# Kernel tuning notes

Measured on AMD Instinct MI355X. Metric: run time of the kernel, lower is better.

## Reference

```python
import jax, jax.numpy as jnp
import numpy as np

B, T, DIM = 2, 2048, 1024
HID = 4096
H, KVH, HD = 16, 4, 64
WIN = 512
NORM_EPS = 1e-5
QK_EPS = 1e-6
LS_INIT = 0.01


def setup_inputs() -> dict:
    key = jax.random.key(0)
    ks = jax.random.split(key, 12)
    s = lambda fan_in: 1.0 / np.sqrt(fan_in)
    return {
        "x": jax.random.normal(ks[0], (B, T, DIM), jnp.float32),
        # torch Linear weights are (out, in); y = x @ W.T
        "wq": jax.random.normal(ks[1], (H * HD, DIM), jnp.float32) * s(DIM),
        "wk": jax.random.normal(ks[2], (KVH * HD, DIM), jnp.float32) * s(DIM),
        "wv": jax.random.normal(ks[3], (KVH * HD, DIM), jnp.float32) * s(DIM),
        "wo": jax.random.normal(ks[4], (DIM, H * HD), jnp.float32) * s(H * HD),
        "w1": jax.random.normal(ks[5], (HID, DIM), jnp.float32) * s(DIM),
        "w2": jax.random.normal(ks[6], (DIM, HID), jnp.float32) * s(HID),
        "w3": jax.random.normal(ks[7], (HID, DIM), jnp.float32) * s(DIM),
        "q_norm_w": jnp.ones((HD,), jnp.float32),
        "k_norm_w": jnp.ones((HD,), jnp.float32),
        "attn_norm_w": jnp.ones((DIM,), jnp.float32),
        "ffn_norm_w": jnp.ones((DIM,), jnp.float32),
        "attn_scale": jnp.full((DIM,), LS_INIT, jnp.float32),
        "ffn_scale": jnp.full((DIM,), LS_INIT, jnp.float32),
    }


def _rmsnorm(x, w, eps):
    return x * jax.lax.rsqrt(jnp.mean(x * x, axis=-1, keepdims=True) + eps) * w


def _attention(x, wq, wk, wv, wo, q_norm_w, k_norm_w):
    b, t, _ = x.shape
    q = (x @ wq.T).reshape(b, t, H, HD)
    k = (x @ wk.T).reshape(b, t, KVH, HD)
    v = (x @ wv.T).reshape(b, t, KVH, HD)
    q = _rmsnorm(q, q_norm_w, QK_EPS)
    k = _rmsnorm(k, k_norm_w, QK_EPS)
    # GQA: repeat kv heads to H heads
    rep = H // KVH
    k = jnp.repeat(k, rep, axis=2)  # (b,t,H,HD)
    v = jnp.repeat(v, rep, axis=2)
    scale = 1.0 / np.sqrt(HD)
    scores = jnp.einsum("bqhd,bkhd->bhqk", q, k) * scale  # (b,H,t,t)
    row = jnp.arange(t)[:, None]
    col = jnp.arange(t)[None, :]
    mask = (row >= col) & (row - col < WIN)  # (t,t) bool
    scores = jnp.where(mask[None, None], scores, -jnp.inf)
    probs = jax.nn.softmax(scores, axis=-1)
    y = jnp.einsum("bhqk,bkhd->bqhd", probs, v).reshape(b, t, H * HD)
    return y @ wo.T


def reference(x, wq, wk, wv, wo, w1, w2, w3, q_norm_w, k_norm_w,
              attn_norm_w, ffn_norm_w, attn_scale, ffn_scale):
    r = _attention(_rmsnorm(x, attn_norm_w, NORM_EPS), wq, wk, wv, wo,
                   q_norm_w, k_norm_w)
    h = x + r * attn_scale
    hn = _rmsnorm(h, ffn_norm_w, NORM_EPS)
    ffn = (jax.nn.silu(hn @ w1.T) * (hn @ w3.T)) @ w2.T
    return h + ffn * ffn_scale
```

## Files before the change

kernel.cpp:

```cpp
#include <hip/hip_runtime.h>

typedef unsigned short u16;
typedef unsigned int u32;
typedef unsigned char u8;
typedef short bf16x8 __attribute__((ext_vector_type(8)));
typedef float f32x4 __attribute__((ext_vector_type(4)));
typedef float f32x16 __attribute__((ext_vector_type(16)));
typedef int i32x4 __attribute__((ext_vector_type(4)));
typedef int i32x8 __attribute__((ext_vector_type(8)));

#define AS1 __attribute__((address_space(1)))
#define AS3 __attribute__((address_space(3)))

#define B_ 2
#define T_ 2048
#define DIM_ 1024
#define HID_ 4096
#define H_ 16
#define KVH_ 4
#define HD_ 64
#define WIN_ 512

#define SCALE_A 0x7C7C7C7C
#define SCALE_B 0x79797979

__device__ __forceinline__ u16 f2bf(float f) {
    union { float f; u32 u; } v; v.f = f;
    u32 r = v.u + 0x7FFFu + ((v.u >> 16) & 1u);
    return (u16)(r >> 16);
}
__device__ __forceinline__ float bf2f(u32 u) {
    union { u32 u; float f; } v; v.u = u << 16;
    return v.f;
}
__device__ __forceinline__ float4 ld4bf(const u16* p) {
    uint2 u = *(const uint2*)p;
    float4 r;
    r.x = bf2f(u.x & 0xFFFFu); r.y = bf2f(u.x >> 16);
    r.z = bf2f(u.y & 0xFFFFu); r.w = bf2f(u.y >> 16);
    return r;
}
__device__ __forceinline__ void load_lds16(const void* g, void* l) {
    __builtin_amdgcn_global_load_lds((AS1 void*)(g), (AS3 void*)(l), 16, 0, 0);
}

__global__ __launch_bounds__(256) void mega_cvt(const float* __restrict__ wq,
                                                const float* __restrict__ wk,
                                                const float* __restrict__ wv,
                                                const float* __restrict__ wo,
                                                const float* __restrict__ w1,
                                                const float* __restrict__ w3,
                                                const float* __restrict__ w2,
                                                u16* __restrict__ wqkv,
                                                u16* __restrict__ wo_b,
                                                u8* __restrict__ w13_8,
                                                u8* __restrict__ w2_8) {
    int i = blockIdx.x * 256 + threadIdx.x;
    if (i < 655360) {
        const float* s; uint2* dbase; size_t didx;
        if (i < 262144)      { s = wq + (size_t)i * 4; dbase = (uint2*)wqkv; didx = i; }
        else if (i < 327680) { int f = i - 262144; s = wk + (size_t)f * 4; dbase = (uint2*)wqkv; didx = 262144 + f; }
        else if (i < 393216) { int f = i - 327680; s = wv + (size_t)f * 4; dbase = (uint2*)wqkv; didx = 327680 + f; }
        else                 { int f = i - 393216; s = wo + (size_t)f * 4; dbase = (uint2*)wo_b; didx = f; }
        float4 v = *(const float4*)s;
        u32 lo = (u32)f2bf(v.x) | ((u32)f2bf(v.y) << 16);
        u32 hi = (u32)f2bf(v.z) | ((u32)f2bf(v.w) << 16);
        dbase[didx] = make_uint2(lo, hi);
    } else {
        const float* s; u32* dbase; size_t didx;
        if (i < 1703936)      { int f = i - 655360;  int c = f >> 8; int n = (c >> 5) * 64 + (c & 31);
                                s = w1 + (size_t)f * 4; dbase = (u32*)w13_8; didx = (size_t)n * 256 + (f & 255); }
        else if (i < 2752512) { int f = i - 1703936; int c = f >> 8; int n = (c >> 5) * 64 + 32 + (c & 31);
                                s = w3 + (size_t)f * 4; dbase = (u32*)w13_8; didx = (size_t)n * 256 + (f & 255); }
        else                  { int f = i - 2752512; s = w2 + (size_t)f * 4; dbase = (u32*)w2_8; didx = f; }
        float4 v = *(const float4*)s;
        int p = __builtin_amdgcn_cvt_pk_fp8_f32(v.x * 64.f, v.y * 64.f, 0, false);
        p = __builtin_amdgcn_cvt_pk_fp8_f32(v.z * 64.f, v.w * 64.f, p, true);
        dbase[didx] = (u32)p;
    }
}

__global__ __launch_bounds__(256) void rmsnorm_kernel(const float* __restrict__ x,
                                                      const float* __restrict__ w,
                                                      u16* __restrict__ out, float eps) {
    int row = blockIdx.x, tid = threadIdx.x;
    const float4 v = ((const float4*)(x + (size_t)row * DIM_))[tid];
    float ss = v.x * v.x + v.y * v.y + v.z * v.z + v.w * v.w;
#pragma unroll
    for (int m = 1; m < 64; m <<= 1) ss += __shfl_xor(ss, m);
    __shared__ float part[4];
    if ((tid & 63) == 0) part[tid >> 6] = ss;
    __syncthreads();
    float tot = part[0] + part[1] + part[2] + part[3];
    float r = rsqrtf(tot * (1.0f / DIM_) + eps);
    const float4 wv = ((const float4*)w)[tid];
    u32 lo = (u32)f2bf(v.x * r * wv.x) | ((u32)f2bf(v.y * r * wv.y) << 16);
    u32 hi = (u32)f2bf(v.z * r * wv.z) | ((u32)f2bf(v.w * r * wv.w) << 16);
    ((uint2*)(out + (size_t)row * DIM_))[tid] = make_uint2(lo, hi);
}

__global__ __launch_bounds__(256) void fuse_attn_kernel(const float* __restrict__ x,
                                                        const u16* __restrict__ p,
                                                        const float* __restrict__ ascale,
                                                        const float* __restrict__ fnw,
                                                        float* __restrict__ h,
                                                        u8* __restrict__ xn8) {
    int row = blockIdx.x, tid = threadIdx.x;
    const float4 xv = ((const float4*)(x + (size_t)row * DIM_))[tid];
    float4 a0 = ld4bf(p + (size_t)row * DIM_ + tid * 4);
    float4 a1 = ld4bf(p + 4194304 + (size_t)row * DIM_ + tid * 4);
    const float4 sc = ((const float4*)ascale)[tid];
    float4 hv;
    hv.x = xv.x + (a0.x + a1.x) * sc.x;
    hv.y = xv.y + (a0.y + a1.y) * sc.y;
    hv.z = xv.z + (a0.z + a1.z) * sc.z;
    hv.w = xv.w + (a0.w + a1.w) * sc.w;
    ((float4*)(h + (size_t)row * DIM_))[tid] = hv;
    float ss = hv.x * hv.x + hv.y * hv.y + hv.z * hv.z + hv.w * hv.w;
#pragma unroll
    for (int m = 1; m < 64; m <<= 1) ss += __shfl_xor(ss, m);
    __shared__ float part[4];
    if ((tid & 63) == 0) part[tid >> 6] = ss;
    __syncthreads();
    float tot = part[0] + part[1] + part[2] + part[3];
    float r = rsqrtf(tot * (1.0f / DIM_) + 1e-5f) * 8.0f;
    const float4 wv = ((const float4*)fnw)[tid];
    int pk = __builtin_amdgcn_cvt_pk_fp8_f32(hv.x * r * wv.x, hv.y * r * wv.y, 0, false);
    pk = __builtin_amdgcn_cvt_pk_fp8_f32(hv.z * r * wv.z, hv.w * r * wv.w, pk, true);
    ((u32*)xn8)[(size_t)row * 256 + tid] = (u32)pk;
}

__global__ __launch_bounds__(256) void fuse_ffn_kernel(const float* __restrict__ h,
                                                       const u16* __restrict__ p,
                                                       const float* __restrict__ fscale,
                                                       float* __restrict__ out) {
    int row = blockIdx.x, tid = threadIdx.x;
    const float4 hv = ((const float4*)(h + (size_t)row * DIM_))[tid];
    size_t off = (size_t)row * DIM_ + tid * 4;
    float4 a0 = ld4bf(p + off);
    float4 a1 = ld4bf(p + 4194304 + off);
    float4 a2 = ld4bf(p + 8388608 + off);
    float4 a3 = ld4bf(p + 12582912 + off);
    const float4 sc = ((const float4*)fscale)[tid];
    float4 o;
    o.x = hv.x + (a0.x + a1.x + a2.x + a3.x) * sc.x;
    o.y = hv.y + (a0.y + a1.y + a2.y + a3.y) * sc.y;
    o.z = hv.z + (a0.z + a1.z + a2.z + a3.z) * sc.z;
    o.w = hv.w + (a0.w + a1.w + a2.w + a3.w) * sc.w;
    ((float4*)(out + (size_t)row * DIM_))[tid] = o;
}

__global__ __launch_bounds__(256) void qkv_post_kernel(const u16* __restrict__ qkv,
                                                       const float* __restrict__ qw,
                                                       const float* __restrict__ kw,
                                                       u16* __restrict__ Qb,
                                                       u16* __restrict__ Kb,
                                                       u16* __restrict__ Vb) {
    int bt = blockIdx.x;
    int b = bt >> 11, t = bt & (T_ - 1);
    int wave = threadIdx.x >> 6, lane = threadIdx.x & 63;
    const u16* row0 = qkv + (size_t)bt * 1536;
    const u16* row1 = row0 + 6291456;
    float qwl = qw[lane], kwl = kw[lane];
#pragma unroll
    for (int i = 0; i < 4; i++) {
        int h = wave * 4 + i;
        float v = bf2f(row0[h * 64 + lane]) + bf2f(row1[h * 64 + lane]);
        float ss = v * v;
#pragma unroll
        for (int m = 1; m < 64; m <<= 1) ss += __shfl_xor(ss, m);
        float r = rsqrtf(ss * (1.0f / 64.0f) + 1e-6f);
        Qb[(((size_t)(b * H_ + h)) * T_ + t) * HD_ + lane] = f2bf(v * r * qwl);
    }
    {
        float v = bf2f(row0[1024 + wave * 64 + lane]) + bf2f(row1[1024 + wave * 64 + lane]);
        float ss = v * v;
#pragma unroll
        for (int m = 1; m < 64; m <<= 1) ss += __shfl_xor(ss, m);
        float r = rsqrtf(ss * (1.0f / 64.0f) + 1e-6f);
        Kb[(((size_t)(b * KVH_ + wave)) * T_ + t) * HD_ + lane] = f2bf(v * r * kwl);
        float vv = bf2f(row0[1280 + wave * 64 + lane]) + bf2f(row1[1280 + wave * 64 + lane]);
        Vb[(((size_t)(b * KVH_ + wave)) * T_ + t) * HD_ + lane] = f2bf(vv);
    }
}

__global__ __launch_bounds__(256) void vtrans_kernel(const u16* __restrict__ Vb,
                                                     u16* __restrict__ Vt) {
    const int bk = blockIdx.x >> 5;
    const int t0 = (blockIdx.x & 31) * 64;
    const int tid = threadIdx.x;
    __shared__ __align__(16) u16 tile[64][64];
    const u16* src = Vb + ((size_t)bk * T_ + t0) * HD_;
#pragma unroll
    for (int i = 0; i < 2; i++) {
        int g = tid + i * 256;
        int r = g >> 3, c8 = g & 7;
        *(bf16x8*)&tile[r][c8 * 8] = *(const bf16x8*)(src + (size_t)r * HD_ + c8 * 8);
    }
    __syncthreads();
    const int d = tid >> 2, ts = (tid & 3) * 16;
    u16 buf[16];
#pragma unroll
    for (int j = 0; j < 16; j++) buf[j] = tile[ts + j][d];
    u16* dst = Vt + (size_t)bk * HD_ * T_ + (size_t)d * T_ + t0 + ts;
    *(bf16x8*)(dst) = *(const bf16x8*)&buf[0];
    *(bf16x8*)(dst + 8) = *(const bf16x8*)&buf[8];
}

__global__ __launch_bounds__(256) void flash_kernel(const u16* __restrict__ Qb,
                                                    const u16* __restrict__ Kb,
                                                    const u16* __restrict__ Vt,
                                                    u16* __restrict__ Ob) {
    const int b = blockIdx.z, h = blockIdx.y, qt = blockIdx.x;
    const int q0 = qt * 64;
    const int tid = threadIdx.x, wave = tid >> 6, lane = tid & 63;
    const int m = lane & 15, quad = lane >> 4;
    const int kvh = h >> 2;

    __shared__ __align__(16) u16 Ps[4][16 * 72];

    const u16* Qp = Qb + ((size_t)(b * H_ + h) * T_) * HD_;
    const u16* Kp = Kb + ((size_t)(b * KVH_ + kvh) * T_) * HD_;
    const u16* Vp = Vt + ((size_t)(b * KVH_ + kvh) * HD_) * T_;

    const int qlo = q0 + wave * 16;
    const int qrow = qlo + m;
    bf16x8 qa0 = *(const bf16x8*)(Qp + (size_t)qrow * 64 + quad * 8);
    bf16x8 qa1 = *(const bf16x8*)(Qp + (size_t)qrow * 64 + 32 + quad * 8);

    f32x4 o[4] = {};
    float mrun = -1e30f, lrun = 0.f;

    const int kt0 = (qlo >= WIN_) ? ((qlo - (WIN_ - 1)) >> 6) : 0;
    const int kt1 = (qlo + 15) >> 6;

    bf16x8 kf[4][2];
#pragma unroll
    for (int st = 0; st < 4; st++) {
        const u16* kp = Kp + (size_t)(kt0 * 64 + st * 16 + m) * 64 + quad * 8;
        kf[st][0] = *(const bf16x8*)(kp);
        kf[st][1] = *(const bf16x8*)(kp + 32);
    }

    for (int kt = kt0; kt <= kt1; ++kt) {
        const int kbase = kt << 6;
        f32x4 s[4];
#pragma unroll
        for (int st = 0; st < 4; st++) {
            f32x4 z = {0.f, 0.f, 0.f, 0.f};
            z = __builtin_amdgcn_mfma_f32_16x16x32_bf16(kf[st][0], qa0, z, 0, 0, 0);
            z = __builtin_amdgcn_mfma_f32_16x16x32_bf16(kf[st][1], qa1, z, 0, 0, 0);
            s[st] = z;
        }
        bf16x8 vb[4][2];
#pragma unroll
        for (int d = 0; d < 4; d++) {
            const u16* vp = Vp + (size_t)(d * 16 + m) * T_ + kbase + quad * 8;
            vb[d][0] = *(const bf16x8*)(vp);
            vb[d][1] = *(const bf16x8*)(vp + 32);
        }
        if (kt < kt1) {
#pragma unroll
            for (int st = 0; st < 4; st++) {
                const u16* kp = Kp + (size_t)(kbase + 64 + st * 16 + m) * 64 + quad * 8;
                kf[st][0] = *(const bf16x8*)(kp);
                kf[st][1] = *(const bf16x8*)(kp + 32);
            }
        }
        float v[16];
        const bool full = (kbase + 63 <= qlo) && (kbase >= qlo - (WIN_ - 16));
        if (full) {
#pragma unroll
            for (int i = 0; i < 16; i++) v[i] = s[i >> 2][i & 3] * 0.125f;
        } else {
            const int D = qrow - kbase - quad * 4;
#pragma unroll
            for (int st = 0; st < 4; st++)
#pragma unroll
                for (int r = 0; r < 4; r++) {
                    int diff = D - st * 16 - r;
                    v[st * 4 + r] = ((u32)diff < (u32)WIN_) ? s[st][r] * 0.125f : -INFINITY;
                }
        }
        float t0 = fmaxf(fmaxf(fmaxf(v[0], v[1]), fmaxf(v[2], v[3])),
                         fmaxf(fmaxf(v[4], v[5]), fmaxf(v[6], v[7])));
        float t1 = fmaxf(fmaxf(fmaxf(v[8], v[9]), fmaxf(v[10], v[11])),
                         fmaxf(fmaxf(v[12], v[13]), fmaxf(v[14], v[15])));
        float rmax = fmaxf(t0, t1);
        rmax = fmaxf(rmax, __shfl_xor(rmax, 16));
        rmax = fmaxf(rmax, __shfl_xor(rmax, 32));
        float mnew = fmaxf(mrun, rmax);
        float alpha = __expf(mrun - mnew);
        float p[16];
#pragma unroll
        for (int i = 0; i < 16; i++) p[i] = __expf(v[i] - mnew);
        float u0 = ((p[0] + p[1]) + (p[2] + p[3])) + ((p[4] + p[5]) + (p[6] + p[7]));
        float u1 = ((p[8] + p[9]) + (p[10] + p[11])) + ((p[12] + p[13]) + (p[14] + p[15]));
        float psum = u0 + u1;
        psum += __shfl_xor(psum, 16);
        psum += __shfl_xor(psum, 32);
        lrun = lrun * alpha + psum;
        mrun = mnew;
#pragma unroll
        for (int d = 0; d < 4; d++) {
            o[d][0] *= alpha; o[d][1] *= alpha; o[d][2] *= alpha; o[d][3] *= alpha;
        }
#pragma unroll
        for (int st = 0; st < 4; st++) {
            u32 lo = (u32)f2bf(p[st * 4 + 0]) | ((u32)f2bf(p[st * 4 + 1]) << 16);
            u32 hi = (u32)f2bf(p[st * 4 + 2]) | ((u32)f2bf(p[st * 4 + 3]) << 16);
            *(uint2*)&Ps[wave][m * 72 + st * 16 + quad * 4] = make_uint2(lo, hi);
        }
        bf16x8 pa0 = *(const bf16x8*)&Ps[wave][m * 72 + quad * 8];
        bf16x8 pa1 = *(const bf16x8*)&Ps[wave][m * 72 + 32 + quad * 8];
#pragma unroll
        for (int d = 0; d < 4; d++) {
            o[d] = __builtin_amdgcn_mfma_f32_16x16x32_bf16(vb[d][0], pa0, o[d], 0, 0, 0);
            o[d] = __builtin_amdgcn_mfma_f32_16x16x32_bf16(vb[d][1], pa1, o[d], 0, 0, 0);
        }
    }
    float inv = 1.0f / lrun;
    u16* ob = Ob + ((size_t)(b * T_ + qrow)) * (H_ * HD_) + h * HD_;
#pragma unroll
    for (int d = 0; d < 4; d++) {
        u32 lo = (u32)f2bf(o[d][0] * inv) | ((u32)f2bf(o[d][1] * inv) << 16);
        u32 hi = (u32)f2bf(o[d][2] * inv) | ((u32)f2bf(o[d][3] * inv) << 16);
        *(uint2*)(ob + d * 16 + quad * 4) = make_uint2(lo, hi);
    }
}

__global__ __launch_bounds__(256) void gemm_bt(const u16* __restrict__ A,
                                               const u16* __restrict__ Bt,
                                               u16* __restrict__ Cb,
                                               int M, int N, int K, int KS) {
    __shared__ __align__(16) u16 As[2][4096];
    __shared__ __align__(16) u16 Bs[2][4096];
    const int tid = threadIdx.x, wave = tid >> 6, lane = tid & 63;
    const int m = lane & 15, quad = lane >> 4;
    const int m0 = blockIdx.y * 128, n0 = blockIdx.x * 128;
    const int wm = (wave >> 1) * 64, wn = (wave & 1) * 64;
    const int kb = blockIdx.z * KS;
    const int nIter = KS >> 5;
    const int slot = wave * 2;
    const int flat0 = slot * 512 + lane * 8;
    const int row0_ = flat0 >> 5, col0 = flat0 & 31;
    const int flat1 = (slot + 1) * 512 + lane * 8;
    const int row1_ = flat1 >> 5, col1 = flat1 & 31;

    f32x4 acc[4][4] = {};

    load_lds16(A + (size_t)(m0 + row0_) * K + kb + col0, &As[0][slot * 512]);
    load_lds16(Bt + (size_t)(n0 + row0_) * K + kb + col0, &Bs[0][slot * 512]);
    load_lds16(A + (size_t)(m0 + row1_) * K + kb + col1, &As[0][(slot + 1) * 512]);
    load_lds16(Bt + (size_t)(n0 + row1_) * K + kb + col1, &Bs[0][(slot + 1) * 512]);

    for (int it = 0; it < nIter; ++it) {
        __syncthreads();
        const int cur = it & 1;
        if (it + 1 < nIter) {
            const int nb = 1 - cur;
            const int k0 = kb + (it + 1) * 32;
            load_lds16(A + (size_t)(m0 + row0_) * K + k0 + col0, &As[nb][slot * 512]);
            load_lds16(Bt + (size_t)(n0 + row0_) * K + k0 + col0, &Bs[nb][slot * 512]);
            load_lds16(A + (size_t)(m0 + row1_) * K + k0 + col1, &As[nb][(slot + 1) * 512]);
            load_lds16(Bt + (size_t)(n0 + row1_) * K + k0 + col1, &Bs[nb][(slot + 1) * 512]);
        }
        bf16x8 af[4], bfr[4];
#pragma unroll
        for (int i = 0; i < 4; i++) af[i] = *(const bf16x8*)&As[cur][(wm + i * 16 + m) * 32 + quad * 8];
#pragma unroll
        for (int j = 0; j < 4; j++) bfr[j] = *(const bf16x8*)&Bs[cur][(wn + j * 16 + m) * 32 + quad * 8];
#pragma unroll
        for (int i = 0; i < 4; i++)
#pragma unroll
            for (int j = 0; j < 4; j++)
                acc[i][j] = __builtin_amdgcn_mfma_f32_16x16x32_bf16(af[i], bfr[j], acc[i][j], 0, 0, 0);
    }

    u16* Cz = Cb + (size_t)blockIdx.z * M * N;
#pragma unroll
    for (int i = 0; i < 4; i++) {
        int rowb = m0 + wm + i * 16 + quad * 4;
#pragma unroll
        for (int j = 0; j < 4; j++) {
            int col = n0 + wn + j * 16 + m;
#pragma unroll
            for (int r = 0; r < 4; r++)
                Cz[(size_t)(rowb + r) * N + col] = f2bf(acc[i][j][r]);
        }
    }
}

#define MFMA8(a, b, c) __builtin_amdgcn_mfma_scale_f32_32x32x64_f8f6f4(a, b, c, 0, 0, 0, SCALE_A, 0, SCALE_B)
#define WAITBAR(N) asm volatile("s_waitcnt vmcnt(" #N ")\n\ts_barrier" ::: "memory")
#define PHASE_MFMA(I0, I1)                           \
    __builtin_amdgcn_s_setprio(1);                   \
    acc[I0][0] = MFMA8(a0, bf0, acc[I0][0]);         \
    acc[I0][1] = MFMA8(a0, bf1, acc[I0][1]);         \
    acc[I1][0] = MFMA8(a1, bf0, acc[I1][0]);         \
    acc[I1][1] = MFMA8(a1, bf1, acc[I1][1]);         \
    __builtin_amdgcn_s_setprio(0);

template <int MODE>
__global__ __launch_bounds__(512) void gemm_fp8(const u8* __restrict__ A,
                                                const u8* __restrict__ Bt,
                                                u16* __restrict__ Cb,
                                                u8* __restrict__ C8,
                                                int M, int N, int K, int KS) {
    __shared__ __align__(16) u8 As[2][32768];
    __shared__ __align__(16) u8 Bs[2][32768];
    const int tid = threadIdx.x, wave = tid >> 6, lane = tid & 63;
    const int l31 = lane & 31, lh = lane >> 5;
    const int m0 = blockIdx.y * 256, n0 = blockIdx.x * 256;
    const int wm = (wave >> 2) * 128, wn = (wave & 3) * 64;
    const int kb = blockIdx.z * KS;
    const int KT = KS >> 7;

    const int srow = ((wave & 3) << 6) + lane;
    const u8* Asrc = A + (size_t)m0 * K + (size_t)srow * K;
    const u8* Bsrc = Bt + (size_t)n0 * K + (size_t)srow * K;
    const int wv2 = wave >> 2;
    const int ldsW = (wave & 3) << 10;

    auto STAGE = [&](const u8* src, int kk, int ks, u8* lds) {
#pragma unroll
        for (int q = 0; q < 2; q++) {
            const int ch = ks * 4 + wv2 + 2 * q;
            load_lds16(src + kk + ch * 16, lds + (ch << 12) + ldsW);
        }
    };
    auto FRAG = [&](const u8* t, int ks, int row) -> i32x8 {
        const int c0 = ks * 4 + (lh << 1);
        union { i32x4 h[2]; i32x8 v; } u;
        u.h[0] = *(const i32x4*)(t + ((c0 << 8) + row) * 16);
        u.h[1] = *(const i32x4*)(t + (((c0 + 1) << 8) + row) * 16);
        return u.v;
    };

    f32x16 acc[4][2] = {};

    STAGE(Asrc, kb, 0, As[0]);
    STAGE(Bsrc, kb, 0, Bs[0]);
    STAGE(Asrc, kb, 1, As[0]);
    STAGE(Bsrc, kb, 1, Bs[0]);

    for (int kt = 0; kt < KT - 1; ++kt) {
        const int cur = kt & 1, nb = cur ^ 1;
        const u8* Ac = As[cur];
        const u8* Bc = Bs[cur];
        const int kn = kb + (kt + 1) * 128;
        i32x8 bf0, bf1, a0, a1;
        STAGE(Asrc, kn, 0, As[nb]);
        WAITBAR(6);
        bf0 = FRAG(Bc, 0, wn + l31);
        bf1 = FRAG(Bc, 0, wn + 32 + l31);
        a0 = FRAG(Ac, 0, wm + l31);
        a1 = FRAG(Ac, 0, wm + 32 + l31);
        PHASE_MFMA(0, 1)
        STAGE(Bsrc, kn, 0, Bs[nb]);
        a0 = FRAG(Ac, 0, wm + 64 + l31);
        a1 = FRAG(Ac, 0, wm + 96 + l31);
        PHASE_MFMA(2, 3)
        STAGE(Asrc, kn, 1, As[nb]);
        WAITBAR(6);
        bf0 = FRAG(Bc, 1, wn + l31);
        bf1 = FRAG(Bc, 1, wn + 32 + l31);
        a0 = FRAG(Ac, 1, wm + l31);
        a1 = FRAG(Ac, 1, wm + 32 + l31);
        PHASE_MFMA(0, 1)
        STAGE(Bsrc, kn, 1, Bs[nb]);
        a0 = FRAG(Ac, 1, wm + 64 + l31);
        a1 = FRAG(Ac, 1, wm + 96 + l31);
        PHASE_MFMA(2, 3)
    }
    {
        const int cur = (KT - 1) & 1;
        const u8* Ac = As[cur];
        const u8* Bc = Bs[cur];
        i32x8 bf0, bf1, a0, a1;
        WAITBAR(4);
        bf0 = FRAG(Bc, 0, wn + l31);
        bf1 = FRAG(Bc, 0, wn + 32 + l31);
        a0 = FRAG(Ac, 0, wm + l31);
        a1 = FRAG(Ac, 0, wm + 32 + l31);
        PHASE_MFMA(0, 1)
        a0 = FRAG(Ac, 0, wm + 64 + l31);
        a1 = FRAG(Ac, 0, wm + 96 + l31);
        PHASE_MFMA(2, 3)
        WAITBAR(0);
        bf0 = FRAG(Bc, 1, wn + l31);
        bf1 = FRAG(Bc, 1, wn + 32 + l31);
        a0 = FRAG(Ac, 1, wm + l31);
        a1 = FRAG(Ac, 1, wm + 32 + l31);
        PHASE_MFMA(0, 1)
        a0 = FRAG(Ac, 1, wm + 64 + l31);
        a1 = FRAG(Ac, 1, wm + 96 + l31);
        PHASE_MFMA(2, 3)
    }

    if (MODE == 0) {
        u16* Cz = Cb + (size_t)blockIdx.z * M * N;
#pragma unroll
        for (int i = 0; i < 4; i++)
#pragma unroll
            for (int j = 0; j < 2; j++) {
                int col = n0 + wn + j * 32 + l31;
#pragma unroll
                for (int reg = 0; reg < 16; reg++) {
                    int row = m0 + wm + i * 32 + (reg & 3) + 8 * (reg >> 2) + 4 * lh;
                    Cz[(size_t)row * N + col] = f2bf(acc[i][j][reg]);
                }
            }
    } else {
        int c = (n0 >> 1) + (wn >> 1) + l31;
#pragma unroll
        for (int i = 0; i < 4; i++)
#pragma unroll
            for (int reg = 0; reg < 16; reg++) {
                int row = m0 + wm + i * 32 + (reg & 3) + 8 * (reg >> 2) + 4 * lh;
                float g1 = acc[i][0][reg], g3 = acc[i][1][reg];
                float res = (g1 / (1.f + __expf(-g1))) * g3 * 8.0f;
                int p = __builtin_amdgcn_cvt_pk_fp8_f32(res, res, 0, false);
                C8[(size_t)row * (N >> 1) + c] = (u8)(p & 0xFF);
            }
    }
}

extern "C" void kernel_launch(void* const* d_in, const int* in_sizes, int n_in,
                              void* d_out, int out_size, void* d_ws, size_t ws_size,
                              hipStream_t stream) {
    const float* x = (const float*)d_in[0];
    const float* wq = (const float*)d_in[1];
    const float* wk = (const float*)d_in[2];
    const float* wv = (const float*)d_in[3];
    const float* wo = (const float*)d_in[4];
    const float* w1 = (const float*)d_in[5];
    const float* w2 = (const float*)d_in[6];
    const float* w3 = (const float*)d_in[7];
    const float* qnw = (const float*)d_in[8];
    const float* knw = (const float*)d_in[9];
    const float* anw = (const float*)d_in[10];
    const float* fnw = (const float*)d_in[11];
    const float* ascale = (const float*)d_in[12];
    const float* fscale = (const float*)d_in[13];
    float* out = (float*)d_out;

    char* ws = (char*)d_ws;
    u16* wqkv_bf = (u16*)(ws + 0);
    u16* wo_bf = (u16*)(ws + 3145728);
    u8* w13_8 = (u8*)(ws + 5242880);
    u8* w2_8 = (u8*)(ws + 13631488);
    u16* xn_bf = (u16*)(ws + 17825792);
    u8* xn8 = (u8*)(ws + 26214400);
    float* h_f = (float*)(ws + 30408704);
    char* P = ws + 47185920;
    u16* qkv_part = (u16*)(P + 0);
    u16* Qb = (u16*)(P + 25165824);
    u16* Kb = (u16*)(P + 33554432);
    u16* Vb = (u16*)(P + 35651584);
    u16* att_bf = (u16*)(P + 37748736);
    u16* Vt = (u16*)(P + 46137344);
    u16* wo_part = (u16*)(P + 0);
    u8* gsw8 = (u8*)(P + 16777216);
    u16* w2_part = (u16*)(P + 33554432);

    mega_cvt<<<14848, 256, 0, stream>>>(wq, wk, wv, wo, w1, w3, w2,
                                        wqkv_bf, wo_bf, w13_8, w2_8);
    rmsnorm_kernel<<<4096, 256, 0, stream>>>(x, anw, xn_bf, 1e-5f);
    gemm_bt<<<dim3(12, 32, 2), 256, 0, stream>>>(xn_bf, wqkv_bf, qkv_part,
                                                 4096, 1536, 1024, 512);
    qkv_post_kernel<<<4096, 256, 0, stream>>>(qkv_part, qnw, knw, Qb, Kb, Vb);
    vtrans_kernel<<<256, 256, 0, stream>>>(Vb, Vt);
    flash_kernel<<<dim3(32, 16, 2), 256, 0, stream>>>(Qb, Kb, Vt, att_bf);
    gemm_bt<<<dim3(8, 32, 2), 256, 0, stream>>>(att_bf, wo_bf, wo_part,
                                                4096, 1024, 1024, 512);
    fuse_attn_kernel<<<4096, 256, 0, stream>>>(x, wo_part, ascale, fnw, h_f, xn8);
    gemm_fp8<1><<<dim3(32, 16, 1), 512, 0, stream>>>(xn8, w13_8, nullptr, gsw8,
                                                     4096, 8192, 1024, 1024);
    gemm_fp8<0><<<dim3(4, 16, 4), 512, 0, stream>>>(gsw8, w2_8, w2_part, nullptr,
                                                    4096, 1024, 4096, 1024);
    fuse_ffn_kernel<<<4096, 256, 0, stream>>>(h_f, w2_part, fscale, out);
}
```

Baseline: 355.7 us.

## Share K/V tiles across GQA heads in flash attention via double-buffered LDS

The flash kernel now launches one block per KV head and query tile. Eight waves cover the 4 query heads sharing that KV head times 2 query halves, and K/V tiles are staged once into swizzled LDS with async global-to-LDS loads, double-buffered. Before, each query-head block reloaded K and V straight from global memory into registers. This is meant to cut redundant K/V traffic by the GQA factor and overlap loads with compute. The costs are fewer blocks (256 vs 1024), a barrier every tile, and each wave looping over a slightly wider key range with per-subtile skip checks.

```diff
diff --git a/kernel.cpp b/kernel.cpp
--- a/kernel.cpp
+++ b/kernel.cpp
@@ -43,6 +43,7 @@
 __device__ __forceinline__ void load_lds16(const void* g, void* l) {
     __builtin_amdgcn_global_load_lds((AS1 void*)(g), (AS3 void*)(l), 16, 0, 0);
 }
+#define WAITBAR(N) asm volatile("s_waitcnt vmcnt(" #N ")\n\ts_barrier" ::: "memory")
 
 __global__ __launch_bounds__(256) void mega_cvt(const float* __restrict__ wq,
                                                 const float* __restrict__ wk,
@@ -207,125 +208,148 @@
     *(bf16x8*)(dst + 8) = *(const bf16x8*)&buf[8];
 }
 
-__global__ __launch_bounds__(256) void flash_kernel(const u16* __restrict__ Qb,
-                                                    const u16* __restrict__ Kb,
-                                                    const u16* __restrict__ Vt,
-                                                    u16* __restrict__ Ob) {
-    const int b = blockIdx.z, h = blockIdx.y, qt = blockIdx.x;
+__global__ __launch_bounds__(512, 2) void flash_kernel(const u16* __restrict__ Qb,
+                                                       const u16* __restrict__ Kb,
+                                                       const u16* __restrict__ Vt,
+                                                       u16* __restrict__ Ob) {
+    const int b = blockIdx.z, kvh = blockIdx.y, qt = blockIdx.x;
     const int q0 = qt * 64;
     const int tid = threadIdx.x, wave = tid >> 6, lane = tid & 63;
+    const int head = wave & 3, qhalf = wave >> 2;
+    const int h = kvh * 4 + head;
     const int m = lane & 15, quad = lane >> 4;
-    const int kvh = h >> 2;
-
-    __shared__ __align__(16) u16 Ps[4][16 * 72];
+
+    __shared__ __align__(16) u16 Ks[2][4096];
+    __shared__ __align__(16) u16 Vs[2][4096];
+    __shared__ __align__(16) u16 Ps[8][16 * 72];
 
     const u16* Qp = Qb + ((size_t)(b * H_ + h) * T_) * HD_;
     const u16* Kp = Kb + ((size_t)(b * KVH_ + kvh) * T_) * HD_;
     const u16* Vp = Vt + ((size_t)(b * KVH_ + kvh) * HD_) * T_;
 
-    const int qlo = q0 + wave * 16;
-    const int qrow = qlo + m;
-    bf16x8 qa0 = *(const bf16x8*)(Qp + (size_t)qrow * 64 + quad * 8);
-    bf16x8 qa1 = *(const bf16x8*)(Qp + (size_t)qrow * 64 + 32 + quad * 8);
-
-    f32x4 o[4] = {};
-    float mrun = -1e30f, lrun = 0.f;
-
-    const int kt0 = (qlo >= WIN_) ? ((qlo - (WIN_ - 1)) >> 6) : 0;
-    const int kt1 = (qlo + 15) >> 6;
-
-    bf16x8 kf[4][2];
-#pragma unroll
-    for (int st = 0; st < 4; st++) {
-        const u16* kp = Kp + (size_t)(kt0 * 64 + st * 16 + m) * 64 + quad * 8;
-        kf[st][0] = *(const bf16x8*)(kp);
-        kf[st][1] = *(const bf16x8*)(kp + 32);
-    }
+    const int qbase = q0 + qhalf * 32;
+    bf16x8 qa[2][2];
+#pragma unroll
+    for (int qs = 0; qs < 2; qs++) {
+        const u16* qp = Qp + (size_t)(qbase + qs * 16 + m) * 64 + quad * 8;
+        qa[qs][0] = *(const bf16x8*)(qp);
+        qa[qs][1] = *(const bf16x8*)(qp + 32);
+    }
+
+    f32x4 o[2][4] = {};
+    float mrun[2] = {-1e30f, -1e30f}, lrun[2] = {0.f, 0.f};
+
+    const int kt0 = (q0 >= WIN_) ? ((q0 - (WIN_ - 1)) >> 6) : 0;
+    const int kt1 = qt;
+
+    const int srow = tid >> 3;
+    const int schunk = (tid & 7) ^ (srow & 7);
+    const u16* Ksrc = Kp + (size_t)srow * 64 + schunk * 8;
+    const u16* Vsrc = Vp + (size_t)srow * T_ + schunk * 8;
+    const int ldsOff = wave * 512;
+
+    load_lds16(Ksrc + (size_t)kt0 * 4096, &Ks[0][ldsOff]);
+    load_lds16(Vsrc + kt0 * 64, &Vs[0][ldsOff]);
 
     for (int kt = kt0; kt <= kt1; ++kt) {
         const int kbase = kt << 6;
-        f32x4 s[4];
+        const int cur = (kt - kt0) & 1;
+        if (kt < kt1) {
+            load_lds16(Ksrc + (size_t)(kt + 1) * 4096, &Ks[cur ^ 1][ldsOff]);
+            load_lds16(Vsrc + (kt + 1) * 64, &Vs[cur ^ 1][ldsOff]);
+            WAITBAR(2);
+        } else {
+            WAITBAR(0);
+        }
+        bf16x8 kf[4][2], vb[4][2];
 #pragma unroll
         for (int st = 0; st < 4; st++) {
-            f32x4 z = {0.f, 0.f, 0.f, 0.f};
-            z = __builtin_amdgcn_mfma_f32_16x16x32_bf16(kf[st][0], qa0, z, 0, 0, 0);
-            z = __builtin_amdgcn_mfma_f32_16x16x32_bf16(kf[st][1], qa1, z, 0, 0, 0);
-            s[st] = z;
-        }
-        bf16x8 vb[4][2];
-#pragma unroll
-        for (int d = 0; d < 4; d++) {
-            const u16* vp = Vp + (size_t)(d * 16 + m) * T_ + kbase + quad * 8;
-            vb[d][0] = *(const bf16x8*)(vp);
-            vb[d][1] = *(const bf16x8*)(vp + 32);
-        }
-        if (kt < kt1) {
-#pragma unroll
-            for (int st = 0; st < 4; st++) {
-                const u16* kp = Kp + (size_t)(kbase + 64 + st * 16 + m) * 64 + quad * 8;
-                kf[st][0] = *(const bf16x8*)(kp);
-                kf[st][1] = *(const bf16x8*)(kp + 32);
+            const int r64 = (st * 16 + m) * 64;
+#pragma unroll
+            for (int hf = 0; hf < 2; hf++) {
+                const int c = (((hf << 2) + quad) ^ (m & 7)) * 8;
+                kf[st][hf] = *(const bf16x8*)&Ks[cur][r64 + c];
+                vb[st][hf] = *(const bf16x8*)&Vs[cur][r64 + c];
             }
         }
-        float v[16];
-        const bool full = (kbase + 63 <= qlo) && (kbase >= qlo - (WIN_ - 16));
-        if (full) {
-#pragma unroll
-            for (int i = 0; i < 16; i++) v[i] = s[i >> 2][i & 3] * 0.125f;
-        } else {
-            const int D = qrow - kbase - quad * 4;
-#pragma unroll
-            for (int st = 0; st < 4; st++)
-#pragma unroll
-                for (int r = 0; r < 4; r++) {
-                    int diff = D - st * 16 - r;
-                    v[st * 4 + r] = ((u32)diff < (u32)WIN_) ? s[st][r] * 0.125f : -INFINITY;
+#pragma unroll
+        for (int qs = 0; qs < 2; qs++) {
+            const int qlo_s = qbase + qs * 16;
+            if (kbase <= qlo_s + 15 && kbase >= qlo_s - 574) {
+                f32x4 s4[4];
+#pragma unroll
+                for (int st = 0; st < 4; st++) {
+                    f32x4 z = {0.f, 0.f, 0.f, 0.f};
+                    z = __builtin_amdgcn_mfma_f32_16x16x32_bf16(kf[st][0], qa[qs][0], z, 0, 0, 0);
+                    z = __builtin_amdgcn_mfma_f32_16x16x32_bf16(kf[st][1], qa[qs][1], z, 0, 0, 0);
+                    s4[st] = z;
                 }
+                float v[16];
+                const bool full = (kbase + 63 <= qlo_s) && (kbase >= qlo_s - 496);
+                if (full) {
+#pragma unroll
+                    for (int i = 0; i < 16; i++) v[i] = s4[i >> 2][i & 3] * 0.125f;
+                } else {
+                    const int D = qlo_s + m - kbase - quad * 4;
+#pragma unroll
+                    for (int st = 0; st < 4; st++)
+#pragma unroll
+                        for (int r = 0; r < 4; r++) {
+                            int diff = D - st * 16 - r;
+                            v[st * 4 + r] = ((u32)diff < (u32)WIN_) ? s4[st][r] * 0.125f : -INFINITY;
+                        }
+                }
+                float t0 = fmaxf(fmaxf(fmaxf(v[0], v[1]), fmaxf(v[2], v[3])),
+                                 fmaxf(fmaxf(v[4], v[5]), fmaxf(v[6], v[7])));
+                float t1 = fmaxf(fmaxf(fmaxf(v[8], v[9]), fmaxf(v[10], v[11])),
+                                 fmaxf(fmaxf(v[12], v[13]), fmaxf(v[14], v[15])));
+                float rmax = fmaxf(t0, t1);
+                rmax = fmaxf(rmax, __shfl_xor(rmax, 16));
+                rmax = fmaxf(rmax, __shfl_xor(rmax, 32));
+                float mnew = fmaxf(mrun[qs], rmax);
+                float alpha = __expf(mrun[qs] - mnew);
+                float p[16];
+#pragma unroll
+                for (int i = 0; i < 16; i++) p[i] = __expf(v[i] - mnew);
+                float u0 = ((p[0] + p[1]) + (p[2] + p[3])) + ((p[4] + p[5]) + (p[6] + p[7]));
+                float u1 = ((p[8] + p[9]) + (p[10] + p[11])) + ((p[12] + p[13]) + (p[14] + p[15]));
+                float psum = u0 + u1;
+                psum += __shfl_xor(psum, 16);
+                psum += __shfl_xor(psum, 32);
+                lrun[qs] = lrun[qs] * alpha + psum;
+                mrun[qs] = mnew;
+#pragma unroll
+                for (int d = 0; d < 4; d++) {
+                    o[qs][d][0] *= alpha; o[qs][d][1] *= alpha;
+                    o[qs][d][2] *= alpha; o[qs][d][3] *= alpha;
+                }
+#pragma unroll
+                for (int st = 0; st < 4; st++) {
+                    u32 lo = (u32)f2bf(p[st * 4 + 0]) | ((u32)f2bf(p[st * 4 + 1]) << 16);
+                    u32 hi = (u32)f2bf(p[st * 4 + 2]) | ((u32)f2bf(p[st * 4 + 3]) << 16);
+                    *(uint2*)&Ps[wave][m * 72 + st * 16 + quad * 4] = make_uint2(lo, hi);
+                }
+                bf16x8 pa0 = *(const bf16x8*)&Ps[wave][m * 72 + quad * 8];
+                bf16x8 pa1 = *(const bf16x8*)&Ps[wave][m * 72 + 32 + quad * 8];
+#pragma unroll
+                for (int d = 0; d < 4; d++) {
+                    o[qs][d] = __builtin_amdgcn_mfma_f32_16x16x32_bf16(vb[d][0], pa0, o[qs][d], 0, 0, 0);
+                    o[qs][d] = __builtin_amdgcn_mfma_f32_16x16x32_bf16(vb[d][1], pa1, o[qs][d], 0, 0, 0);
+                }
+            }
         }
-        float t0 = fmaxf(fmaxf(fmaxf(v[0], v[1]), fmaxf(v[2], v[3])),
-                         fmaxf(fmaxf(v[4], v[5]), fmaxf(v[6], v[7])));
-        float t1 = fmaxf(fmaxf(fmaxf(v[8], v[9]), fmaxf(v[10], v[11])),
-                         fmaxf(fmaxf(v[12], v[13]), fmaxf(v[14], v[15])));
-        float rmax = fmaxf(t0, t1);
-        rmax = fmaxf(rmax, __shfl_xor(rmax, 16));
-        rmax = fmaxf(rmax, __shfl_xor(rmax, 32));
-        float mnew = fmaxf(mrun, rmax);
-        float alpha = __expf(mrun - mnew);
-        float p[16];
-#pragma unroll
-        for (int i = 0; i < 16; i++) p[i] = __expf(v[i] - mnew);
-        float u0 = ((p[0] + p[1]) + (p[2] + p[3])) + ((p[4] + p[5]) + (p[6] + p[7]));
-        float u1 = ((p[8] + p[9]) + (p[10] + p[11])) + ((p[12] + p[13]) + (p[14] + p[15]));
-        float psum = u0 + u1;
-        psum += __shfl_xor(psum, 16);
-        psum += __shfl_xor(psum, 32);
-        lrun = lrun * alpha + psum;
-        mrun = mnew;
+        asm volatile("s_barrier" ::: "memory");
+    }
+#pragma unroll
+    for (int qs = 0; qs < 2; qs++) {
+        float inv = 1.0f / lrun[qs];
+        u16* ob = Ob + ((size_t)(b * T_ + qbase + qs * 16 + m)) * (H_ * HD_) + h * HD_;
 #pragma unroll
         for (int d = 0; d < 4; d++) {
-            o[d][0] *= alpha; o[d][1] *= alpha; o[d][2] *= alpha; o[d][3] *= alpha;
+            u32 lo = (u32)f2bf(o[qs][d][0] * inv) | ((u32)f2bf(o[qs][d][1] * inv) << 16);
+            u32 hi = (u32)f2bf(o[qs][d][2] * inv) | ((u32)f2bf(o[qs][d][3] * inv) << 16);
+            *(uint2*)(ob + d * 16 + quad * 4) = make_uint2(lo, hi);
         }
-#pragma unroll
-        for (int st = 0; st < 4; st++) {
-            u32 lo = (u32)f2bf(p[st * 4 + 0]) | ((u32)f2bf(p[st * 4 + 1]) << 16);
-            u32 hi = (u32)f2bf(p[st * 4 + 2]) | ((u32)f2bf(p[st * 4 + 3]) << 16);
-            *(uint2*)&Ps[wave][m * 72 + st * 16 + quad * 4] = make_uint2(lo, hi);
-        }
-        bf16x8 pa0 = *(const bf16x8*)&Ps[wave][m * 72 + quad * 8];
-        bf16x8 pa1 = *(const bf16x8*)&Ps[wave][m * 72 + 32 + quad * 8];
-#pragma unroll
-        for (int d = 0; d < 4; d++) {
-            o[d] = __builtin_amdgcn_mfma_f32_16x16x32_bf16(vb[d][0], pa0, o[d], 0, 0, 0);
-            o[d] = __builtin_amdgcn_mfma_f32_16x16x32_bf16(vb[d][1], pa1, o[d], 0, 0, 0);
-        }
-    }
-    float inv = 1.0f / lrun;
-    u16* ob = Ob + ((size_t)(b * T_ + qrow)) * (H_ * HD_) + h * HD_;
-#pragma unroll
-    for (int d = 0; d < 4; d++) {
-        u32 lo = (u32)f2bf(o[d][0] * inv) | ((u32)f2bf(o[d][1] * inv) << 16);
-        u32 hi = (u32)f2bf(o[d][2] * inv) | ((u32)f2bf(o[d][3] * inv) << 16);
-        *(uint2*)(ob + d * 16 + quad * 4) = make_uint2(lo, hi);
     }
 }
 
@@ -392,7 +416,6 @@
 }
 
 #define MFMA8(a, b, c) __builtin_amdgcn_mfma_scale_f32_32x32x64_f8f6f4(a, b, c, 0, 0, 0, SCALE_A, 0, SCALE_B)
-#define WAITBAR(N) asm volatile("s_waitcnt vmcnt(" #N ")\n\ts_barrier" ::: "memory")
 #define PHASE_MFMA(I0, I1)                           \
     __builtin_amdgcn_s_setprio(1);                   \
     acc[I0][0] = MFMA8(a0, bf0, acc[I0][0]);         \
@@ -571,7 +594,7 @@
                                                  4096, 1536, 1024, 512);
     qkv_post_kernel<<<4096, 256, 0, stream>>>(qkv_part, qnw, knw, Qb, Kb, Vb);
     vtrans_kernel<<<256, 256, 0, stream>>>(Vb, Vt);
-    flash_kernel<<<dim3(32, 16, 2), 256, 0, stream>>>(Qb, Kb, Vt, att_bf);
+    flash_kernel<<<dim3(32, KVH_, B_), 512, 0, stream>>>(Qb, Kb, Vt, att_bf);
     gemm_bt<<<dim3(8, 32, 2), 256, 0, stream>>>(att_bf, wo_bf, wo_part,
                                                 4096, 1024, 1024, 512);
     fuse_attn_kernel<<<4096, 256, 0, stream>>>(x, wo_part, ascale, fnw, h_f, xn8);
```

Measured after the change: 319.7 us. -10.1%, faster.
